# Kernel optimization log

Measured on AMD Instinct MI355X. Metric: run time of the kernel, lower is better.

## Reference

```python
import jax, jax.numpy as jnp
import numpy as np

N_NODES = 50000

def sage_conv(x, src, dst, W_l, b_l, W_r):
    # mean-aggregate neighbor features x[src] at dst, then lin_l(agg)+lin_r(x)
    msgs = x[src]                                       # [E, d]
    agg = jax.ops.segment_sum(msgs, dst, num_segments=N_NODES)
    cnt = jax.ops.segment_sum(jnp.ones((src.shape[0],), x.dtype), dst, num_segments=N_NODES)
    agg = agg / jnp.maximum(cnt, 1.0)[:, None]          # [N, d]
    return agg @ W_l.T + b_l + x @ W_r.T


def setup_inputs() -> dict:
    key = jax.random.key(0)
    ks = jax.random.split(key, 10)
    in_c, hid, out_c = 128, 128, 64
    x = jax.random.normal(ks[0], (N_NODES, in_c), dtype=jnp.float32)
    edge_index = jax.random.randint(ks[1], (2, 800000), 0, N_NODES, dtype=jnp.int64)
    s = 1.0 / np.sqrt(in_c)
    W1_l = jax.random.uniform(ks[2], (hid, in_c), minval=-s, maxval=s)
    b1 = jax.random.uniform(ks[3], (hid,), minval=-s, maxval=s)
    W1_r = jax.random.uniform(ks[4], (hid, in_c), minval=-s, maxval=s)
    s = 1.0 / np.sqrt(hid)
    W2_l = jax.random.uniform(ks[5], (hid, hid), minval=-s, maxval=s)
    b2 = jax.random.uniform(ks[6], (hid,), minval=-s, maxval=s)
    W2_r = jax.random.uniform(ks[7], (hid, hid), minval=-s, maxval=s)
    W3 = jax.random.uniform(ks[8], (out_c, hid), minval=-s, maxval=s)
    b3 = jax.random.uniform(ks[9], (out_c,), minval=-s, maxval=s)
    return {"x": x, "edge_index": edge_index, "W1_l": W1_l, "b1": b1, "W1_r": W1_r,
            "W2_l": W2_l, "b2": b2, "W2_r": W2_r, "W3": W3, "b3": b3}


def reference(x, edge_index, W1_l, b1, W1_r, W2_l, b2, W2_r, W3, b3):
    src, dst = edge_index[0], edge_index[1]
    h = jax.nn.relu(sage_conv(x, src, dst, W1_l, b1, W1_r))
    h = jax.nn.relu(sage_conv(h, src, dst, W2_l, b2, W2_r))
    return h @ W3.T + b3
```

## Files before the change

kernel.cpp:

```cpp
#include <hip/hip_runtime.h>

#define FDIM 128

typedef __attribute__((ext_vector_type(8))) short bf16x8;
typedef __attribute__((ext_vector_type(4))) float f32x4;

static __device__ __forceinline__ ushort f2bf(float f) {
    uint u = __float_as_uint(f);
    uint r = (u + 0x7FFF + ((u >> 16) & 1)) >> 16;
    return (ushort)r;
}
static __device__ __forceinline__ uint packbf(float lo, float hi) {
    return (uint)f2bf(lo) | ((uint)f2bf(hi) << 16);
}
static __device__ __forceinline__ float bflo(uint v) { return __uint_as_float(v << 16); }
static __device__ __forceinline__ float bfhi(uint v) { return __uint_as_float(v & 0xFFFF0000u); }


__global__ void prep_kernel(const float* __restrict__ x, ushort* __restrict__ xb, int nx8,
                            const float* __restrict__ W1l, const float* __restrict__ W1r,
                            const float* __restrict__ W2l, const float* __restrict__ W2r,
                            const float* __restrict__ W3, ushort* __restrict__ wbuf,
                            const int* __restrict__ dst, int E, int* __restrict__ bcnt,
                            int nconv) {
    const int b = blockIdx.x;
    const int tid = threadIdx.x;
    if (b < nconv) {
        int i = b * 256 + tid;
        if (i < nx8) {
            const float* s = x + (size_t)i * 8;
            float4 a = *(const float4*)(s);
            float4 c = *(const float4*)(s + 4);
            uint4 o;
            o.x = packbf(a.x, a.y); o.y = packbf(a.z, a.w);
            o.z = packbf(c.x, c.y); o.w = packbf(c.z, c.w);
            *(uint4*)(xb + (size_t)i * 8) = o;
        }
    } else if (b < nconv + 36) {
        int c = (b - nconv) * 256 + tid;
        const float* s; ushort* d;
        if (c < 2048)      { s = W1l + (size_t)c * 8;          d = wbuf + (size_t)c * 8; }
        else if (c < 4096) { s = W1r + (size_t)(c - 2048) * 8; d = wbuf + 16384 + (size_t)(c - 2048) * 8; }
        else if (c < 6144) { s = W2l + (size_t)(c - 4096) * 8; d = wbuf + 32768 + (size_t)(c - 4096) * 8; }
        else if (c < 8192) { s = W2r + (size_t)(c - 6144) * 8; d = wbuf + 49152 + (size_t)(c - 6144) * 8; }
        else               { s = W3  + (size_t)(c - 8192) * 8; d = wbuf + 65536 + (size_t)(c - 8192) * 8; }
        float4 a = *(const float4*)(s);
        float4 cc = *(const float4*)(s + 4);
        uint4 o;
        o.x = packbf(a.x, a.y); o.y = packbf(a.z, a.w);
        o.z = packbf(cc.x, cc.y); o.w = packbf(cc.z, cc.w);
        *(uint4*)d = o;
    } else {
        __shared__ int lh[256];
        int hb = b - nconv - 36;
        lh[tid] = 0;
        __syncthreads();
        #pragma unroll
        for (int k = 0; k < 8; ++k) {
            int e = hb * 2048 + k * 256 + tid;
            if (e < E) atomicAdd(&lh[dst[e] >> 8], 1);
        }
        __syncthreads();
        if (lh[tid]) atomicAdd(&bcnt[tid], lh[tid]);
    }
}


__global__ void scan_buckets(const int* __restrict__ bcnt, int* __restrict__ bbase,
                             int* __restrict__ bcur, int nb) {
    const int lane = threadIdx.x;
    const int i0 = lane * 4;
    int v0 = (i0 + 0 < nb) ? bcnt[i0 + 0] : 0;
    int v1 = (i0 + 1 < nb) ? bcnt[i0 + 1] : 0;
    int v2 = (i0 + 2 < nb) ? bcnt[i0 + 2] : 0;
    int v3 = (i0 + 3 < nb) ? bcnt[i0 + 3] : 0;
    int s = v0 + v1 + v2 + v3;
    int incl = s;
    #pragma unroll
    for (int d = 1; d < 64; d <<= 1) {
        int t = __shfl_up(incl, d);
        if (lane >= d) incl += t;
    }
    int excl = incl - s;
    int e0 = excl, e1 = excl + v0, e2 = e1 + v1, e3 = e2 + v2;
    if (i0 + 0 < nb) { bbase[i0 + 0] = e0; bcur[i0 + 0] = e0; }
    if (i0 + 1 < nb) { bbase[i0 + 1] = e1; bcur[i0 + 1] = e1; }
    if (i0 + 2 < nb) { bbase[i0 + 2] = e2; bcur[i0 + 2] = e2; }
    if (i0 + 3 < nb) { bbase[i0 + 3] = e3; bcur[i0 + 3] = e3; }
    int total = __shfl(incl, 63);
    if (lane == 0) bbase[nb] = total;
}


__global__ void pair_scatter(const int* __restrict__ src, const int* __restrict__ dst,
                             int* __restrict__ bcur, uint* __restrict__ pairs, int E) {
    __shared__ int lh[256];
    __shared__ int gb[256];
    const int tid = threadIdx.x;
    lh[tid] = 0;
    __syncthreads();
    int ss[8], dd[8], sl[8];
    #pragma unroll
    for (int k = 0; k < 8; ++k) {
        int e = blockIdx.x * 2048 + k * 256 + tid;
        if (e < E) {
            ss[k] = src[e];
            dd[k] = dst[e];
            sl[k] = atomicAdd(&lh[dd[k] >> 8], 1);
        } else dd[k] = -1;
    }
    __syncthreads();
    if (lh[tid]) gb[tid] = atomicAdd(&bcur[tid], lh[tid]);
    __syncthreads();
    #pragma unroll
    for (int k = 0; k < 8; ++k) {
        if (dd[k] >= 0)
            pairs[gb[dd[k] >> 8] + sl[k]] = (uint)ss[k] | ((uint)(dd[k] & 255) << 24);
    }
}


__global__ void bucket_csr(const uint* __restrict__ pairs, const int* __restrict__ bbase,
                           int* __restrict__ off, int* __restrict__ csr, int N) {
    __shared__ int cnt[256];
    __shared__ int base[256];
    __shared__ int cur[256];
    const int b = blockIdx.x;
    const int tid = threadIdx.x;
    const int p0 = bbase[b], p1 = bbase[b + 1];
    cnt[tid] = 0;
    __syncthreads();
    for (int p = p0 + tid; p < p1; p += 256) atomicAdd(&cnt[pairs[p] >> 24], 1);
    __syncthreads();
    if (tid < 64) {
        int i0 = tid * 4;
        int v0 = cnt[i0], v1 = cnt[i0 + 1], v2 = cnt[i0 + 2], v3 = cnt[i0 + 3];
        int s = v0 + v1 + v2 + v3;
        int incl = s;
        #pragma unroll
        for (int d = 1; d < 64; d <<= 1) {
            int t = __shfl_up(incl, d);
            if (tid >= d) incl += t;
        }
        int excl = incl - s;
        base[i0] = excl; base[i0 + 1] = excl + v0;
        base[i0 + 2] = excl + v0 + v1; base[i0 + 3] = excl + v0 + v1 + v2;
        cur[i0] = base[i0]; cur[i0 + 1] = base[i0 + 1];
        cur[i0 + 2] = base[i0 + 2]; cur[i0 + 3] = base[i0 + 3];
    }
    __syncthreads();
    int node = (b << 8) + tid;
    if (node <= N) off[node] = p0 + base[tid];
    for (int p = p0 + tid; p < p1; p += 256) {
        uint e = pairs[p];
        int slot = atomicAdd(&cur[e >> 24], 1);
        csr[p0 + slot] = (int)(e & 0xFFFFFF);
    }
}


template<int HEAD>
__global__ void fused_sage(const ushort* __restrict__ feat, const int* __restrict__ off,
                           const int* __restrict__ csr,
                           const ushort* __restrict__ Wl, const ushort* __restrict__ Wr,
                           const float* __restrict__ bias,
                           const ushort* __restrict__ W3, const float* __restrict__ b3,
                           ushort* __restrict__ hout, float* __restrict__ fout, int n) {
    __shared__ __align__(16) ushort As[32 * FDIM];
    __shared__ __align__(16) ushort Xs[32 * FDIM];
    const int row0 = blockIdx.x * 32;
    const int lane = threadIdx.x & 63;
    const int wid  = threadIdx.x >> 6;

    const float4 z4 = make_float4(0.f, 0.f, 0.f, 0.f);
    #pragma unroll
    for (int i = 0; i < 2; ++i) {
        int s = threadIdx.x + i * 256;
        int r = s >> 4, cch = s & 15;
        int row = row0 + r;
        float4 vx = (row < n) ? *(const float4*)(feat + (size_t)row * FDIM + cch * 8) : z4;
        *(float4*)(Xs + (r * 16 + (cch ^ (r & 7))) * 8) = vx;
    }

    const int g = lane >> 4;
    const int c = lane & 15;
    for (int i = 0; i < 8; ++i) {
        const int r = wid * 8 + i;
        const int node = row0 + r;
        float a[8] = {0.f, 0.f, 0.f, 0.f, 0.f, 0.f, 0.f, 0.f};
        float inv = 0.f;
        if (node < n) {
            const int j0 = off[node], j1 = off[node + 1];
            int j = j0 + g;
            for (; j + 12 < j1; j += 16) {
                int s0 = csr[j], s1 = csr[j + 4], s2 = csr[j + 8], s3 = csr[j + 12];
                uint4 v0 = *(const uint4*)(feat + (size_t)s0 * FDIM + c * 8);
                uint4 v1 = *(const uint4*)(feat + (size_t)s1 * FDIM + c * 8);
                uint4 v2 = *(const uint4*)(feat + (size_t)s2 * FDIM + c * 8);
                uint4 v3 = *(const uint4*)(feat + (size_t)s3 * FDIM + c * 8);
                a[0] += bflo(v0.x) + bflo(v1.x) + bflo(v2.x) + bflo(v3.x);
                a[1] += bfhi(v0.x) + bfhi(v1.x) + bfhi(v2.x) + bfhi(v3.x);
                a[2] += bflo(v0.y) + bflo(v1.y) + bflo(v2.y) + bflo(v3.y);
                a[3] += bfhi(v0.y) + bfhi(v1.y) + bfhi(v2.y) + bfhi(v3.y);
                a[4] += bflo(v0.z) + bflo(v1.z) + bflo(v2.z) + bflo(v3.z);
                a[5] += bfhi(v0.z) + bfhi(v1.z) + bfhi(v2.z) + bfhi(v3.z);
                a[6] += bflo(v0.w) + bflo(v1.w) + bflo(v2.w) + bflo(v3.w);
                a[7] += bfhi(v0.w) + bfhi(v1.w) + bfhi(v2.w) + bfhi(v3.w);
            }
            for (; j + 4 < j1; j += 8) {
                int s0 = csr[j], s1 = csr[j + 4];
                uint4 v0 = *(const uint4*)(feat + (size_t)s0 * FDIM + c * 8);
                uint4 v1 = *(const uint4*)(feat + (size_t)s1 * FDIM + c * 8);
                a[0] += bflo(v0.x) + bflo(v1.x); a[1] += bfhi(v0.x) + bfhi(v1.x);
                a[2] += bflo(v0.y) + bflo(v1.y); a[3] += bfhi(v0.y) + bfhi(v1.y);
                a[4] += bflo(v0.z) + bflo(v1.z); a[5] += bfhi(v0.z) + bfhi(v1.z);
                a[6] += bflo(v0.w) + bflo(v1.w); a[7] += bfhi(v0.w) + bfhi(v1.w);
            }
            for (; j < j1; j += 4) {
                int s0 = csr[j];
                uint4 v0 = *(const uint4*)(feat + (size_t)s0 * FDIM + c * 8);
                a[0] += bflo(v0.x); a[1] += bfhi(v0.x);
                a[2] += bflo(v0.y); a[3] += bfhi(v0.y);
                a[4] += bflo(v0.z); a[5] += bfhi(v0.z);
                a[6] += bflo(v0.w); a[7] += bfhi(v0.w);
            }
            inv = 1.0f / fmaxf((float)(j1 - j0), 1.0f);
        }
        #pragma unroll
        for (int k = 0; k < 8; ++k) {
            a[k] += __shfl_xor(a[k], 16);
            a[k] += __shfl_xor(a[k], 32);
        }
        if (g == 0) {
            uint4 o;
            o.x = packbf(a[0] * inv, a[1] * inv);
            o.y = packbf(a[2] * inv, a[3] * inv);
            o.z = packbf(a[4] * inv, a[5] * inv);
            o.w = packbf(a[6] * inv, a[7] * inv);
            *(uint4*)(As + (r * 16 + (c ^ (r & 7))) * 8) = o;
        }
    }
    __syncthreads();

    const int wrow = wid & 1;
    const int wcol = wid >> 1;
    const int lr = lane & 15;
    const int lk = lane >> 4;

    f32x4 acc[4];
    #pragma unroll
    for (int t = 0; t < 4; ++t) acc[t] = (f32x4){0.f, 0.f, 0.f, 0.f};

    const int arow = wrow * 16 + lr;
    #pragma unroll
    for (int ks = 0; ks < 4; ++ks) {
        bf16x8 a = *(const bf16x8*)(As + (arow * 16 + ((ks * 4 + lk) ^ (arow & 7))) * 8);
        #pragma unroll
        for (int t = 0; t < 4; ++t) {
            int wr = wcol * 64 + t * 16 + lr;
            bf16x8 bb = *(const bf16x8*)(Wl + (size_t)wr * FDIM + ks * 32 + lk * 8);
            acc[t] = __builtin_amdgcn_mfma_f32_16x16x32_bf16(a, bb, acc[t], 0, 0, 0);
        }
    }
    #pragma unroll
    for (int ks = 0; ks < 4; ++ks) {
        bf16x8 a = *(const bf16x8*)(Xs + (arow * 16 + ((ks * 4 + lk) ^ (arow & 7))) * 8);
        #pragma unroll
        for (int t = 0; t < 4; ++t) {
            int wr = wcol * 64 + t * 16 + lr;
            bf16x8 bb = *(const bf16x8*)(Wr + (size_t)wr * FDIM + ks * 32 + lk * 8);
            acc[t] = __builtin_amdgcn_mfma_f32_16x16x32_bf16(a, bb, acc[t], 0, 0, 0);
        }
    }

    if (HEAD == 0) {
        #pragma unroll
        for (int t = 0; t < 4; ++t) {
            int col = wcol * 64 + t * 16 + lr;
            float bc = bias[col];
            #pragma unroll
            for (int j = 0; j < 4; ++j) {
                int row = row0 + wrow * 16 + lk * 4 + j;
                if (row < n) {
                    float v = fmaxf(acc[t][j] + bc, 0.f);
                    hout[(size_t)row * FDIM + col] = f2bf(v);
                }
            }
        }
    } else {
        __syncthreads();
        #pragma unroll
        for (int t = 0; t < 4; ++t) {
            int col = wcol * 64 + t * 16 + lr;
            float bc = bias[col];
            #pragma unroll
            for (int j = 0; j < 4; ++j) {
                int r = wrow * 16 + lk * 4 + j;
                float v = fmaxf(acc[t][j] + bc, 0.f);
                As[(r * 16 + ((col >> 3) ^ (r & 7))) * 8 + (col & 7)] = f2bf(v);
            }
        }
        __syncthreads();

        f32x4 acc2[2];
        #pragma unroll
        for (int t = 0; t < 2; ++t) acc2[t] = (f32x4){0.f, 0.f, 0.f, 0.f};

        #pragma unroll
        for (int ks = 0; ks < 4; ++ks) {
            bf16x8 a = *(const bf16x8*)(As + (arow * 16 + ((ks * 4 + lk) ^ (arow & 7))) * 8);
            #pragma unroll
            for (int t = 0; t < 2; ++t) {
                int wr = wcol * 32 + t * 16 + lr;
                bf16x8 bb = *(const bf16x8*)(W3 + (size_t)wr * FDIM + ks * 32 + lk * 8);
                acc2[t] = __builtin_amdgcn_mfma_f32_16x16x32_bf16(a, bb, acc2[t], 0, 0, 0);
            }
        }

        #pragma unroll
        for (int t = 0; t < 2; ++t) {
            int col = wcol * 32 + t * 16 + lr;
            float bc = b3[col];
            #pragma unroll
            for (int j = 0; j < 4; ++j) {
                int row = row0 + wrow * 16 + lk * 4 + j;
                if (row < n) fout[(size_t)row * 64 + col] = acc2[t][j] + bc;
            }
        }
    }
}


extern "C" void kernel_launch(void* const* d_in, const int* in_sizes, int n_in,
                              void* d_out, int out_size, void* d_ws, size_t ws_size,
                              hipStream_t stream) {
    const float* x   = (const float*)d_in[0];
    const int*   ei  = (const int*)d_in[1];
    const float* W1l = (const float*)d_in[2];
    const float* b1  = (const float*)d_in[3];
    const float* W1r = (const float*)d_in[4];
    const float* W2l = (const float*)d_in[5];
    const float* b2  = (const float*)d_in[6];
    const float* W2r = (const float*)d_in[7];
    const float* W3  = (const float*)d_in[8];
    const float* b3  = (const float*)d_in[9];
    float* out = (float*)d_out;

    const int N = in_sizes[0] / FDIM;
    const int E = in_sizes[1] / 2;
    const int* src = ei;
    const int* dst = ei + E;
    const int NBK = (N + 255) >> 8;

    char* ws = (char*)d_ws;
    size_t p = 0;
    auto alloc = [&](size_t bytes) {
        char* q = ws + p;
        p += (bytes + 255) & ~(size_t)255;
        return q;
    };
    int* bcnt    = (int*)alloc(256 * 4);
    int* bbase   = (int*)alloc(260 * 4);
    int* bcur    = (int*)alloc(256 * 4);
    uint* pairs  = (uint*)alloc((size_t)E * 4);
    int* csr     = (int*)alloc((size_t)E * 4);
    int* off     = (int*)alloc((size_t)(N + 1) * 4);
    ushort* xb   = (ushort*)alloc((size_t)N * FDIM * 2);
    ushort* h1b  = (ushort*)alloc((size_t)N * FDIM * 2);
    ushort* wbuf = (ushort*)alloc(73728 * 2);
    ushort* w1l = wbuf, *w1r = wbuf + 16384, *w2l = wbuf + 32768,
           *w2r = wbuf + 49152, *w3 = wbuf + 65536;

    hipMemsetAsync(bcnt, 0, 256 * 4, stream);

    const int nx8   = N * FDIM / 8;
    const int nconv = (nx8 + 255) / 256;
    const int nhist = (E + 2047) / 2048;
    prep_kernel<<<nconv + 36 + nhist, 256, 0, stream>>>(
        x, xb, nx8, W1l, W1r, W2l, W2r, W3, wbuf, dst, E, bcnt, nconv);
    scan_buckets<<<1, 64, 0, stream>>>(bcnt, bbase, bcur, NBK);
    pair_scatter<<<(E + 2047) / 2048, 256, 0, stream>>>(src, dst, bcur, pairs, E);
    bucket_csr<<<NBK, 256, 0, stream>>>(pairs, bbase, off, csr, N);

    const int lgrid = (N + 31) / 32;
    fused_sage<0><<<lgrid, 256, 0, stream>>>(xb, off, csr, w1l, w1r, b1,
                                             (const ushort*)nullptr, (const float*)nullptr,
                                             h1b, (float*)nullptr, N);
    fused_sage<1><<<lgrid, 256, 0, stream>>>(h1b, off, csr, w2l, w2r, b2,
                                             w3, b3, (ushort*)nullptr, out, N);
}
```

Measured before the change: 169.7 us.

## Fuse bucket scan into histogram via last-block pattern; interleave two-row gathers

The separate single-block scan kernel is removed. The last histogram block, detected through an atomic done-counter, now performs the bucket prefix scan, saving one kernel launch. In fused_sage each wave preloads its row offsets once and distributes them with shuffles, replacing per-row loads. It then aggregates two destination rows at once with interleaved gathers to raise memory-level parallelism, at the cost of more registers and tail loops.

```diff
diff --git a/kernel.cpp b/kernel.cpp
--- a/kernel.cpp
+++ b/kernel.cpp
@@ -15,6 +15,12 @@
 }
 static __device__ __forceinline__ float bflo(uint v) { return __uint_as_float(v << 16); }
 static __device__ __forceinline__ float bfhi(uint v) { return __uint_as_float(v & 0xFFFF0000u); }
+
+#define ACC8(A, V) do { \
+    A[0] += bflo((V).x); A[1] += bfhi((V).x); \
+    A[2] += bflo((V).y); A[3] += bfhi((V).y); \
+    A[4] += bflo((V).z); A[5] += bfhi((V).z); \
+    A[6] += bflo((V).w); A[7] += bfhi((V).w); } while (0)
 
 
 __global__ void prep_kernel(const float* __restrict__ x, ushort* __restrict__ xb, int nx8,
@@ -22,7 +28,8 @@
                             const float* __restrict__ W2l, const float* __restrict__ W2r,
                             const float* __restrict__ W3, ushort* __restrict__ wbuf,
                             const int* __restrict__ dst, int E, int* __restrict__ bcnt,
-                            int nconv) {
+                            int* __restrict__ hdone, int* __restrict__ bbase,
+                            int* __restrict__ bcur, int nb, int nconv, int nhist) {
     const int b = blockIdx.x;
     const int tid = threadIdx.x;
     if (b < nconv) {
@@ -52,6 +59,7 @@
         *(uint4*)d = o;
     } else {
         __shared__ int lh[256];
+        __shared__ int isLast;
         int hb = b - nconv - 36;
         lh[tid] = 0;
         __syncthreads();
@@ -62,33 +70,37 @@
         }
         __syncthreads();
         if (lh[tid]) atomicAdd(&bcnt[tid], lh[tid]);
-    }
-}
-
-
-__global__ void scan_buckets(const int* __restrict__ bcnt, int* __restrict__ bbase,
-                             int* __restrict__ bcur, int nb) {
-    const int lane = threadIdx.x;
-    const int i0 = lane * 4;
-    int v0 = (i0 + 0 < nb) ? bcnt[i0 + 0] : 0;
-    int v1 = (i0 + 1 < nb) ? bcnt[i0 + 1] : 0;
-    int v2 = (i0 + 2 < nb) ? bcnt[i0 + 2] : 0;
-    int v3 = (i0 + 3 < nb) ? bcnt[i0 + 3] : 0;
-    int s = v0 + v1 + v2 + v3;
-    int incl = s;
-    #pragma unroll
-    for (int d = 1; d < 64; d <<= 1) {
-        int t = __shfl_up(incl, d);
-        if (lane >= d) incl += t;
-    }
-    int excl = incl - s;
-    int e0 = excl, e1 = excl + v0, e2 = e1 + v1, e3 = e2 + v2;
-    if (i0 + 0 < nb) { bbase[i0 + 0] = e0; bcur[i0 + 0] = e0; }
-    if (i0 + 1 < nb) { bbase[i0 + 1] = e1; bcur[i0 + 1] = e1; }
-    if (i0 + 2 < nb) { bbase[i0 + 2] = e2; bcur[i0 + 2] = e2; }
-    if (i0 + 3 < nb) { bbase[i0 + 3] = e3; bcur[i0 + 3] = e3; }
-    int total = __shfl(incl, 63);
-    if (lane == 0) bbase[nb] = total;
+        __syncthreads();
+        if (tid == 0) {
+            __threadfence();
+            isLast = (atomicAdd(hdone, 1) == nhist - 1);
+        }
+        __syncthreads();
+        if (isLast && tid < 64) {
+            __threadfence();
+            volatile int* vb = bcnt;
+            const int i0 = tid * 4;
+            int v0 = (i0 + 0 < nb) ? vb[i0 + 0] : 0;
+            int v1 = (i0 + 1 < nb) ? vb[i0 + 1] : 0;
+            int v2 = (i0 + 2 < nb) ? vb[i0 + 2] : 0;
+            int v3 = (i0 + 3 < nb) ? vb[i0 + 3] : 0;
+            int s = v0 + v1 + v2 + v3;
+            int incl = s;
+            #pragma unroll
+            for (int d = 1; d < 64; d <<= 1) {
+                int t = __shfl_up(incl, d);
+                if (tid >= d) incl += t;
+            }
+            int excl = incl - s;
+            int e0 = excl, e1 = excl + v0, e2 = e1 + v1, e3 = e2 + v2;
+            if (i0 + 0 < nb) { bbase[i0 + 0] = e0; bcur[i0 + 0] = e0; }
+            if (i0 + 1 < nb) { bbase[i0 + 1] = e1; bcur[i0 + 1] = e1; }
+            if (i0 + 2 < nb) { bbase[i0 + 2] = e2; bcur[i0 + 2] = e2; }
+            if (i0 + 3 < nb) { bbase[i0 + 3] = e3; bcur[i0 + 3] = e3; }
+            int total = __shfl(incl, 63);
+            if (tid == 0) bbase[nb] = total;
+        }
+    }
 }
 
 
@@ -172,6 +184,8 @@
     const int lane = threadIdx.x & 63;
     const int wid  = threadIdx.x >> 6;
 
+    const int offv = off[min(row0 + wid * 8 + min(lane, 8), n)];
+
     const float4 z4 = make_float4(0.f, 0.f, 0.f, 0.f);
     #pragma unroll
     for (int i = 0; i < 2; ++i) {
@@ -184,62 +198,79 @@
 
     const int g = lane >> 4;
     const int c = lane & 15;
-    for (int i = 0; i < 8; ++i) {
-        const int r = wid * 8 + i;
-        const int node = row0 + r;
+    #define LDROW(s) (*(const uint4*)(feat + (size_t)(s) * FDIM + c * 8))
+
+    #pragma unroll
+    for (int i = 0; i < 4; ++i) {
+        const int rA = wid * 8 + 2 * i;
+        const int nodeA = row0 + rA, nodeB = nodeA + 1;
+        const int j0A = __shfl(offv, 2 * i), j1A = __shfl(offv, 2 * i + 1);
+        const int j1B = __shfl(offv, 2 * i + 2);
         float a[8] = {0.f, 0.f, 0.f, 0.f, 0.f, 0.f, 0.f, 0.f};
-        float inv = 0.f;
-        if (node < n) {
-            const int j0 = off[node], j1 = off[node + 1];
-            int j = j0 + g;
-            for (; j + 12 < j1; j += 16) {
-                int s0 = csr[j], s1 = csr[j + 4], s2 = csr[j + 8], s3 = csr[j + 12];
-                uint4 v0 = *(const uint4*)(feat + (size_t)s0 * FDIM + c * 8);
-                uint4 v1 = *(const uint4*)(feat + (size_t)s1 * FDIM + c * 8);
-                uint4 v2 = *(const uint4*)(feat + (size_t)s2 * FDIM + c * 8);
-                uint4 v3 = *(const uint4*)(feat + (size_t)s3 * FDIM + c * 8);
-                a[0] += bflo(v0.x) + bflo(v1.x) + bflo(v2.x) + bflo(v3.x);
-                a[1] += bfhi(v0.x) + bfhi(v1.x) + bfhi(v2.x) + bfhi(v3.x);
-                a[2] += bflo(v0.y) + bflo(v1.y) + bflo(v2.y) + bflo(v3.y);
-                a[3] += bfhi(v0.y) + bfhi(v1.y) + bfhi(v2.y) + bfhi(v3.y);
-                a[4] += bflo(v0.z) + bflo(v1.z) + bflo(v2.z) + bflo(v3.z);
-                a[5] += bfhi(v0.z) + bfhi(v1.z) + bfhi(v2.z) + bfhi(v3.z);
-                a[6] += bflo(v0.w) + bflo(v1.w) + bflo(v2.w) + bflo(v3.w);
-                a[7] += bfhi(v0.w) + bfhi(v1.w) + bfhi(v2.w) + bfhi(v3.w);
-            }
-            for (; j + 4 < j1; j += 8) {
-                int s0 = csr[j], s1 = csr[j + 4];
-                uint4 v0 = *(const uint4*)(feat + (size_t)s0 * FDIM + c * 8);
-                uint4 v1 = *(const uint4*)(feat + (size_t)s1 * FDIM + c * 8);
-                a[0] += bflo(v0.x) + bflo(v1.x); a[1] += bfhi(v0.x) + bfhi(v1.x);
-                a[2] += bflo(v0.y) + bflo(v1.y); a[3] += bfhi(v0.y) + bfhi(v1.y);
-                a[4] += bflo(v0.z) + bflo(v1.z); a[5] += bfhi(v0.z) + bfhi(v1.z);
-                a[6] += bflo(v0.w) + bflo(v1.w); a[7] += bfhi(v0.w) + bfhi(v1.w);
-            }
-            for (; j < j1; j += 4) {
-                int s0 = csr[j];
-                uint4 v0 = *(const uint4*)(feat + (size_t)s0 * FDIM + c * 8);
-                a[0] += bflo(v0.x); a[1] += bfhi(v0.x);
-                a[2] += bflo(v0.y); a[3] += bfhi(v0.y);
-                a[4] += bflo(v0.z); a[5] += bfhi(v0.z);
-                a[6] += bflo(v0.w); a[7] += bfhi(v0.w);
-            }
-            inv = 1.0f / fmaxf((float)(j1 - j0), 1.0f);
+        float bacc[8] = {0.f, 0.f, 0.f, 0.f, 0.f, 0.f, 0.f, 0.f};
+        int jA = j0A + g, jB = j1A + g;
+        for (; jA + 12 < j1A && jB + 12 < j1B; jA += 16, jB += 16) {
+            int sA0 = csr[jA], sA1 = csr[jA + 4], sA2 = csr[jA + 8], sA3 = csr[jA + 12];
+            int sB0 = csr[jB], sB1 = csr[jB + 4], sB2 = csr[jB + 8], sB3 = csr[jB + 12];
+            uint4 vA0 = LDROW(sA0), vA1 = LDROW(sA1), vA2 = LDROW(sA2), vA3 = LDROW(sA3);
+            uint4 vB0 = LDROW(sB0), vB1 = LDROW(sB1), vB2 = LDROW(sB2), vB3 = LDROW(sB3);
+            ACC8(a, vA0); ACC8(a, vA1); ACC8(a, vA2); ACC8(a, vA3);
+            ACC8(bacc, vB0); ACC8(bacc, vB1); ACC8(bacc, vB2); ACC8(bacc, vB3);
+        }
+        for (; jA + 12 < j1A; jA += 16) {
+            int s0 = csr[jA], s1 = csr[jA + 4], s2 = csr[jA + 8], s3 = csr[jA + 12];
+            uint4 v0 = LDROW(s0), v1 = LDROW(s1), v2 = LDROW(s2), v3 = LDROW(s3);
+            ACC8(a, v0); ACC8(a, v1); ACC8(a, v2); ACC8(a, v3);
+        }
+        for (; jA + 4 < j1A; jA += 8) {
+            int s0 = csr[jA], s1 = csr[jA + 4];
+            uint4 v0 = LDROW(s0), v1 = LDROW(s1);
+            ACC8(a, v0); ACC8(a, v1);
+        }
+        for (; jA < j1A; jA += 4) {
+            int s0 = csr[jA];
+            uint4 v0 = LDROW(s0);
+            ACC8(a, v0);
+        }
+        for (; jB + 12 < j1B; jB += 16) {
+            int s0 = csr[jB], s1 = csr[jB + 4], s2 = csr[jB + 8], s3 = csr[jB + 12];
+            uint4 v0 = LDROW(s0), v1 = LDROW(s1), v2 = LDROW(s2), v3 = LDROW(s3);
+            ACC8(bacc, v0); ACC8(bacc, v1); ACC8(bacc, v2); ACC8(bacc, v3);
+        }
+        for (; jB + 4 < j1B; jB += 8) {
+            int s0 = csr[jB], s1 = csr[jB + 4];
+            uint4 v0 = LDROW(s0), v1 = LDROW(s1);
+            ACC8(bacc, v0); ACC8(bacc, v1);
+        }
+        for (; jB < j1B; jB += 4) {
+            int s0 = csr[jB];
+            uint4 v0 = LDROW(s0);
+            ACC8(bacc, v0);
         }
         #pragma unroll
         for (int k = 0; k < 8; ++k) {
             a[k] += __shfl_xor(a[k], 16);
+            bacc[k] += __shfl_xor(bacc[k], 16);
             a[k] += __shfl_xor(a[k], 32);
+            bacc[k] += __shfl_xor(bacc[k], 32);
         }
         if (g == 0) {
-            uint4 o;
-            o.x = packbf(a[0] * inv, a[1] * inv);
-            o.y = packbf(a[2] * inv, a[3] * inv);
-            o.z = packbf(a[4] * inv, a[5] * inv);
-            o.w = packbf(a[6] * inv, a[7] * inv);
-            *(uint4*)(As + (r * 16 + (c ^ (r & 7))) * 8) = o;
-        }
-    }
+            float invA = (nodeA < n) ? 1.0f / fmaxf((float)(j1A - j0A), 1.0f) : 0.f;
+            float invB = (nodeB < n) ? 1.0f / fmaxf((float)(j1B - j1A), 1.0f) : 0.f;
+            uint4 oA, oB;
+            oA.x = packbf(a[0] * invA, a[1] * invA);
+            oA.y = packbf(a[2] * invA, a[3] * invA);
+            oA.z = packbf(a[4] * invA, a[5] * invA);
+            oA.w = packbf(a[6] * invA, a[7] * invA);
+            oB.x = packbf(bacc[0] * invB, bacc[1] * invB);
+            oB.y = packbf(bacc[2] * invB, bacc[3] * invB);
+            oB.z = packbf(bacc[4] * invB, bacc[5] * invB);
+            oB.w = packbf(bacc[6] * invB, bacc[7] * invB);
+            *(uint4*)(As + (rA * 16 + (c ^ (rA & 7))) * 8) = oA;
+            *(uint4*)(As + ((rA + 1) * 16 + (c ^ ((rA + 1) & 7))) * 8) = oB;
+        }
+    }
+    #undef LDROW
     __syncthreads();
 
     const int wrow = wid & 1;
@@ -359,7 +390,9 @@
         p += (bytes + 255) & ~(size_t)255;
         return q;
     };
-    int* bcnt    = (int*)alloc(256 * 4);
+    int* ctrl    = (int*)alloc(272 * 4);
+    int* bcnt    = ctrl;
+    int* hdone   = ctrl + 256;
     int* bbase   = (int*)alloc(260 * 4);
     int* bcur    = (int*)alloc(256 * 4);
     uint* pairs  = (uint*)alloc((size_t)E * 4);
@@ -371,14 +404,14 @@
     ushort* w1l = wbuf, *w1r = wbuf + 16384, *w2l = wbuf + 32768,
            *w2r = wbuf + 49152, *w3 = wbuf + 65536;
 
-    hipMemsetAsync(bcnt, 0, 256 * 4, stream);
+    hipMemsetAsync(ctrl, 0, 257 * 4, stream);
 
     const int nx8   = N * FDIM / 8;
     const int nconv = (nx8 + 255) / 256;
     const int nhist = (E + 2047) / 2048;
     prep_kernel<<<nconv + 36 + nhist, 256, 0, stream>>>(
-        x, xb, nx8, W1l, W1r, W2l, W2r, W3, wbuf, dst, E, bcnt, nconv);
-    scan_buckets<<<1, 64, 0, stream>>>(bcnt, bbase, bcur, NBK);
+        x, xb, nx8, W1l, W1r, W2l, W2r, W3, wbuf, dst, E, bcnt,
+        hdone, bbase, bcur, NBK, nconv, nhist);
     pair_scatter<<<(E + 2047) / 2048, 256, 0, stream>>>(src, dst, bcur, pairs, E);
     bucket_csr<<<NBK, 256, 0, stream>>>(pairs, bbase, off, csr, N);
 
```

Result: slower. 199.8 us (+17.8%).
